# Kernel tuning notes

Hardware: AMD Instinct MI355X
Metric: run time of the kernel (lower is better)

Reference implementation:

```python
import jax, jax.numpy as jnp
import numpy as np

D_MODEL = 1024
NUM_HEADS = 16
D_K = D_MODEL // NUM_HEADS


def setup_inputs() -> dict:
    key = jax.random.key(0)
    ks = jax.random.split(key, 9)
    s = 1.0 / np.sqrt(D_MODEL)
    x = jax.random.normal(ks[0], (2, 2048, D_MODEL), dtype=jnp.float32)
    Wq = jax.random.uniform(ks[1], (D_MODEL, D_MODEL), jnp.float32, -s, s)
    bq = jax.random.uniform(ks[2], (D_MODEL,), jnp.float32, -s, s)
    Wk = jax.random.uniform(ks[3], (D_MODEL, D_MODEL), jnp.float32, -s, s)
    bk = jax.random.uniform(ks[4], (D_MODEL,), jnp.float32, -s, s)
    Wv = jax.random.uniform(ks[5], (D_MODEL, D_MODEL), jnp.float32, -s, s)
    bv = jax.random.uniform(ks[6], (D_MODEL,), jnp.float32, -s, s)
    Wo = jax.random.uniform(ks[7], (D_MODEL, D_MODEL), jnp.float32, -s, s)
    bo = jax.random.uniform(ks[8], (D_MODEL,), jnp.float32, -s, s)
    return {"x": x, "Wq": Wq, "bq": bq, "Wk": Wk, "bk": bk,
            "Wv": Wv, "bv": bv, "Wo": Wo, "bo": bo}


def reference(x, Wq, bq, Wk, bk, Wv, bv, Wo, bo):
    B, S, _ = x.shape
    # projections (torch Linear: x @ W.T + b; here W stored as [in, out])
    q = (x @ Wq + bq).reshape(B, S, NUM_HEADS, D_K).transpose(0, 2, 1, 3)
    k = (x @ Wk + bk).reshape(B, S, NUM_HEADS, D_K).transpose(0, 2, 1, 3)
    v = (x @ Wv + bv).reshape(B, S, NUM_HEADS, D_K).transpose(0, 2, 1, 3)
    scores = jnp.einsum('bhqd,bhkd->bhqk', q, k) / jnp.sqrt(jnp.float32(D_K))
    attn = jax.nn.softmax(scores, axis=-1)
    out = jnp.einsum('bhqk,bhkd->bhqd', attn, v)  # [B,H,S,Dk]
    out = out.transpose(0, 2, 1, 3).reshape(B, S, D_MODEL)
    return out @ Wo + bo
```

## Files before the change

kernel.cpp:

```cpp
#include <hip/hip_runtime.h>
#include <hip/hip_bf16.h>

#define SEQ   2048
#define DM    1024
#define NH    16
#define DK    64
#define BATCH 2
#define M_TOT 4096
#define C1 0.18033688011112042f

typedef __attribute__((ext_vector_type(8))) short bf16x8;
typedef __attribute__((ext_vector_type(4))) float f32x4;
typedef __attribute__((ext_vector_type(16))) float f32x16;
typedef __attribute__((ext_vector_type(2))) int i32x2;
typedef unsigned short u16;

__device__ inline u16 f2b(float f) {
    union { float f; unsigned u; } x; x.f = f;
    return (u16)((x.u + 0x7FFFu + ((x.u >> 16) & 1u)) >> 16);
}

__device__ inline unsigned pk2(float a, float b) {
    __hip_bfloat162 h = __float22bfloat162_rn(make_float2(a, b));
    return *reinterpret_cast<unsigned*>(&h);
}

__device__ inline void async_cp16(const u16* g, u16* l) {
    __builtin_amdgcn_global_load_lds(
        (const __attribute__((address_space(1))) unsigned int*)g,
        (__attribute__((address_space(3))) unsigned int*)l, 16, 0, 0);
}

__device__ inline f32x16 zero16() {
    f32x16 z;
    #pragma unroll
    for (int i = 0; i < 16; ++i) z[i] = 0.f;
    return z;
}

__device__ inline bf16x8 mk8(unsigned a, unsigned b, unsigned c, unsigned d) {
    union { unsigned u[4]; bf16x8 v; } x;
    x.u[0] = a; x.u[1] = b; x.u[2] = c; x.u[3] = d;
    return x.v;
}

#define MFMA32(a, b, c) __builtin_amdgcn_mfma_f32_32x32x16_bf16(a, b, c, 0, 0, 0)

__global__ __launch_bounds__(256) void cast_x(
    const float4* __restrict__ x, uint2* __restrict__ xb)
{
    int gid = blockIdx.x * 256 + threadIdx.x;
    float4 v = x[gid];
    uint2 o;
    o.x = pk2(v.x, v.y); o.y = pk2(v.z, v.w);
    xb[gid] = o;
}

__global__ __launch_bounds__(256) void transpose_cast4(
    const float* __restrict__ W0, const float* __restrict__ W1,
    const float* __restrict__ W2, const float* __restrict__ W3,
    u16* __restrict__ WtBase)
{
    __shared__ float tile[32][33];
    const int t = threadIdx.x;
    const int n0 = blockIdx.x << 5, k0 = blockIdx.y << 5, z = blockIdx.z;
    const float* W = (z == 0) ? W0 : (z == 1) ? W1 : (z == 2) ? W2 : W3;
    u16* Wt = WtBase + (size_t)z * DM * DM;
    #pragma unroll
    for (int i = 0; i < 4; ++i) {
        int idx = t + (i << 8); int r = idx >> 5, c = idx & 31;
        tile[r][c] = W[(size_t)(k0 + r) * DM + n0 + c];
    }
    __syncthreads();
    #pragma unroll
    for (int i = 0; i < 4; ++i) {
        int idx = t + (i << 8); int r = idx >> 5, c = idx & 31;
        Wt[(size_t)(n0 + r) * DM + k0 + c] = f2b(tile[c][r]);
    }
}

__global__ __launch_bounds__(256) void gemm_bt(
    const u16* __restrict__ A, const u16* __restrict__ Bt, int mode,
    const float* __restrict__ bias0, const float* __restrict__ bias1,
    const float* __restrict__ bias2,
    void* __restrict__ out0, void* __restrict__ out1, void* __restrict__ out2)
{
    __shared__ u16 sh[16896];
    u16* As = sh;
    u16* Bs = sh + 8192;
    const int t = threadIdx.x, wid = t >> 6, lane = t & 63;
    const int lr = lane & 15, quad = lane >> 4;
    const int m0 = blockIdx.y << 7, n0 = blockIdx.x << 7;
    const int wm = (wid & 1) << 6, wn = (wid >> 1) << 6;
    const int rowA = lane >> 2;
    const int colA = (((lane & 3) - ((lane >> 3) & 3)) & 3) << 3;
    const int sA = (((lr >> 1) + quad) & 3) << 3;

    f32x4 acc[4][4];
    #pragma unroll
    for (int i = 0; i < 4; ++i)
        #pragma unroll
        for (int j = 0; j < 4; ++j) acc[i][j] = (f32x4){0.f, 0.f, 0.f, 0.f};

    auto stage = [&](int k0s, int buf) {
        #pragma unroll
        for (int i = 0; i < 2; ++i) {
            int ch = wid * 2 + i;
            async_cp16(A  + (size_t)(m0 + ch * 16 + rowA) * DM + k0s + colA,
                       As + buf * 4096 + ch * 16 * 32);
            async_cp16(Bt + (size_t)(n0 + ch * 16 + rowA) * DM + k0s + colA,
                       Bs + buf * 4096 + ch * 16 * 32);
        }
    };

    stage(0, 0);
    __syncthreads();

    for (int k0 = 0; k0 < DM; k0 += 32) {
        const int cur = (k0 >> 5) & 1;
        if (k0 + 32 < DM) stage(k0 + 32, cur ^ 1);

        const u16* Ac = As + cur * 4096;
        const u16* Bc = Bs + cur * 4096;
        bf16x8 af[4], bfr[4];
        #pragma unroll
        for (int mt = 0; mt < 4; ++mt)
            af[mt] = *(const bf16x8*)(Ac + (wm + 16 * mt + lr) * 32 + sA);
        #pragma unroll
        for (int nt = 0; nt < 4; ++nt)
            bfr[nt] = *(const bf16x8*)(Bc + (wn + 16 * nt + lr) * 32 + sA);
        #pragma unroll
        for (int mt = 0; mt < 4; ++mt)
            #pragma unroll
            for (int nt = 0; nt < 4; ++nt)
                acc[mt][nt] = __builtin_amdgcn_mfma_f32_16x16x32_bf16(
                    af[mt], bfr[nt], acc[mt][nt], 0, 0, 0);
        __syncthreads();
    }

    if (mode == 1) {
        u16* wstrip = sh + wid * 1152;
        const int ngb = n0 + wn;
        const int which = ngb >> 10, nnb = ngb & 1023;
        const int h = nnb >> 6;
        const float* bp = (which == 0) ? bias0 : (which == 1) ? bias1 : bias2;
        const float sc = (which == 0) ? C1 : 1.0f;
        float bias_v[4];
        #pragma unroll
        for (int nt = 0; nt < 4; ++nt) bias_v[nt] = bp[nnb + 16 * nt + lr];

        if (which != 1) {
            u16* dst = (which == 0) ? (u16*)out0 : (u16*)out2;
            #pragma unroll
            for (int mt = 0; mt < 4; ++mt) {
                #pragma unroll
                for (int nt = 0; nt < 4; ++nt) {
                    uint2 w;
                    w.x = pk2((acc[mt][nt][0] + bias_v[nt]) * sc,
                              (acc[mt][nt][1] + bias_v[nt]) * sc);
                    w.y = pk2((acc[mt][nt][2] + bias_v[nt]) * sc,
                              (acc[mt][nt][3] + bias_v[nt]) * sc);
                    *(uint2*)(wstrip + (16 * nt + lr) * 16 + quad * 4) = w;
                }
                asm volatile("s_waitcnt lgkmcnt(0)" ::: "memory");
                #pragma unroll
                for (int half = 0; half < 2; ++half) {
                    int id = lane + 64 * half;
                    int d = id >> 1, cho = (id & 1) << 3;
                    int m = m0 + wm + 16 * mt + cho;
                    int b = m >> 11, s = m & (SEQ - 1);
                    *(uint4*)(dst + ((size_t)(b * NH + h) * DK + d) * SEQ + s) =
                        *(const uint4*)(wstrip + d * 16 + cho);
                }
                asm volatile("s_waitcnt lgkmcnt(0)" ::: "memory");
            }
        } else {
            u16* dst = (u16*)out1;
            #pragma unroll
            for (int mt = 0; mt < 4; ++mt) {
                #pragma unroll
                for (int nt = 0; nt < 4; ++nt)
                    #pragma unroll
                    for (int r = 0; r < 4; ++r)
                        wstrip[(quad * 4 + r) * 72 + 16 * nt + lr] =
                            f2b(acc[mt][nt][r] + bias_v[nt]);
                asm volatile("s_waitcnt lgkmcnt(0)" ::: "memory");
                #pragma unroll
                for (int half = 0; half < 2; ++half) {
                    int id = lane + 64 * half;
                    int mloc = id >> 3, dl = (id & 7) << 3;
                    int m = m0 + wm + 16 * mt + mloc;
                    int b = m >> 11, s = m & (SEQ - 1);
                    *(uint4*)(dst + ((size_t)(b * NH + h) * SEQ + s) * DK + dl) =
                        *(const uint4*)(wstrip + mloc * 72 + dl);
                }
                asm volatile("s_waitcnt lgkmcnt(0)" ::: "memory");
            }
        }
    } else {
        float* O = (float*)out0;
        float* strip = (float*)sh + wid * 1088;
        float bias_v[4];
        #pragma unroll
        for (int nt = 0; nt < 4; ++nt) bias_v[nt] = bias0[n0 + wn + 16 * nt + lr];
        #pragma unroll
        for (int mt = 0; mt < 4; ++mt) {
            #pragma unroll
            for (int nt = 0; nt < 4; ++nt)
                #pragma unroll
                for (int r = 0; r < 4; ++r)
                    strip[(quad * 4 + r) * 68 + 16 * nt + lr] =
                        acc[mt][nt][r] + bias_v[nt];
            asm volatile("s_waitcnt lgkmcnt(0)" ::: "memory");
            #pragma unroll
            for (int rr = 0; rr < 4; ++rr) {
                int row = lane >> 2, chunk = (lane & 3) + 4 * rr;
                float4 v = *(const float4*)(strip + row * 68 + chunk * 4);
                *(float4*)(O + (size_t)(m0 + wm + 16 * mt + row) * DM
                             + n0 + wn + chunk * 4) = v;
            }
            asm volatile("s_waitcnt lgkmcnt(0)" ::: "memory");
        }
    }
}

__global__ __launch_bounds__(512) void attn_mfma(
    const u16* __restrict__ Qt, const u16* __restrict__ K,
    const u16* __restrict__ Vt, u16* __restrict__ A)
{
    __shared__ u16 sh[33280];

    const int t = threadIdx.x, wid = t >> 6, lane = t & 63;
    const int l31 = lane & 31, hi = lane >> 5, l7 = lane & 7;
    const int g = wid >> 2, wq = wid & 3;
    const int bx = blockIdx.x;
    const int xcd = bx & 7, within = bx >> 3;
    const int bh  = xcd * 4 + (within >> 4);
    const int q0  = (within & 15) << 7;

    const u16* Kb = K  + (size_t)bh * SEQ * DK;
    const u16* Vb = Vt + (size_t)bh * DK * SEQ;

    const int qw = q0 + 32 * wq + l31;
    const u16* Qb = Qt + (size_t)bh * DK * SEQ + qw;
    bf16x8 bQ[4];
    #pragma unroll
    for (int s = 0; s < 4; ++s)
        #pragma unroll
        for (int j = 0; j < 8; ++j)
            bQ[s][j] = (short)Qb[(size_t)(16 * s + 8 * hi + j) * SEQ];

    f32x16 O0 = zero16(), O1 = zero16();
    float lr = 0.f;

    const int w8row = wid * 8 + (lane >> 3);
    const int scol  = ((l7 ^ (lane >> 3)) << 3);

    const int rA = l31 * 64;
    int cks[4];
    #pragma unroll
    for (int s = 0; s < 4; ++s) cks[s] = ((2 * s + hi) ^ l7) << 3;

    auto stage = [&](int sit, int buf) {
        const int kt = sit << 7;
        u16* kd = sh + (buf << 13) + wid * 512;
        u16* vd = sh + 16384 + (buf << 13) + wid * 512;
        async_cp16(Kb + (size_t)(kt + w8row) * DK + scol,       kd);
        async_cp16(Kb + (size_t)(kt + 64 + w8row) * DK + scol,  kd + 4096);
        async_cp16(Vb + (size_t)w8row * SEQ + kt + scol,        vd);
        async_cp16(Vb + (size_t)w8row * SEQ + kt + 64 + scol,   vd + 4096);
    };

    stage(0, 0);
    __syncthreads();

    for (int sit = 0; sit < SEQ / 128; ++sit) {
        const u16* kbp = sh + ((sit & 1) << 13) + (g << 12) + rA;
        const u16* vbp = sh + 16384 + ((sit & 1) << 13) + (g << 12) + rA;
        if (sit + 1 < SEQ / 128) stage(sit + 1, (sit + 1) & 1);

        f32x16 Sv[2];
        __builtin_amdgcn_s_setprio(1);
        {
            bf16x8 a;
            Sv[0] = zero16();
            a = *(const bf16x8*)(kbp + cks[0]); Sv[0] = MFMA32(a, bQ[0], Sv[0]);
            a = *(const bf16x8*)(kbp + cks[1]); Sv[0] = MFMA32(a, bQ[1], Sv[0]);
            a = *(const bf16x8*)(kbp + cks[2]); Sv[0] = MFMA32(a, bQ[2], Sv[0]);
            a = *(const bf16x8*)(kbp + cks[3]); Sv[0] = MFMA32(a, bQ[3], Sv[0]);
            Sv[1] = zero16();
            a = *(const bf16x8*)(kbp + 2048 + cks[0]); Sv[1] = MFMA32(a, bQ[0], Sv[1]);
            a = *(const bf16x8*)(kbp + 2048 + cks[1]); Sv[1] = MFMA32(a, bQ[1], Sv[1]);
            a = *(const bf16x8*)(kbp + 2048 + cks[2]); Sv[1] = MFMA32(a, bQ[2], Sv[1]);
            a = *(const bf16x8*)(kbp + 2048 + cks[3]); Sv[1] = MFMA32(a, bQ[3], Sv[1]);
        }
        __builtin_amdgcn_s_setprio(0);

        unsigned pa[4][4];
        #pragma unroll
        for (int kvt = 0; kvt < 2; ++kvt) {
            float e[16];
            #pragma unroll
            for (int r = 0; r < 16; ++r)
                e[r] = __builtin_amdgcn_exp2f(Sv[kvt][r]);
            lr += (((e[0] + e[1]) + (e[2] + e[3])) +
                   ((e[4] + e[5]) + (e[6] + e[7]))) +
                  (((e[8] + e[9]) + (e[10] + e[11])) +
                   ((e[12] + e[13]) + (e[14] + e[15])));
            unsigned pk8[8];
            #pragma unroll
            for (int i = 0; i < 8; ++i) pk8[i] = pk2(e[2 * i], e[2 * i + 1]);
            #pragma unroll
            for (int ww = 0; ww < 2; ++ww) {
                i32x2 r0 = __builtin_amdgcn_permlane32_swap(
                    (int)pk8[4 * ww + 0], (int)pk8[4 * ww + 2], false, false);
                i32x2 r1 = __builtin_amdgcn_permlane32_swap(
                    (int)pk8[4 * ww + 1], (int)pk8[4 * ww + 3], false, false);
                const int w = 2 * kvt + ww;
                pa[w][0] = (unsigned)r0[0]; pa[w][1] = (unsigned)r1[0];
                pa[w][2] = (unsigned)r0[1]; pa[w][3] = (unsigned)r1[1];
            }
        }

        __builtin_amdgcn_s_setprio(1);
        #pragma unroll
        for (int w = 0; w < 4; ++w) {
            bf16x8 pw = mk8(pa[w][0], pa[w][1], pa[w][2], pa[w][3]);
            bf16x8 v0 = *(const bf16x8*)(vbp + cks[w]);
            bf16x8 v1 = *(const bf16x8*)(vbp + 2048 + cks[w]);
            O0 = MFMA32(pw, v0, O0);
            O1 = MFMA32(pw, v1, O1);
        }
        __builtin_amdgcn_s_setprio(0);

        __syncthreads();
    }

    lr += __shfl_xor(lr, 32);

    float* lred = (float*)(sh + 32768);
    if (g == 1) {
        float* red = (float*)sh + wq * 2048;
        #pragma unroll
        for (int c = 0; c < 4; ++c) {
            float4 v0 = make_float4(O0[4*c], O0[4*c+1], O0[4*c+2], O0[4*c+3]);
            float4 v1 = make_float4(O1[4*c], O1[4*c+1], O1[4*c+2], O1[4*c+3]);
            *(float4*)(red + lane * 32 + ((c ^ l7) << 2))       = v0;
            *(float4*)(red + lane * 32 + (((c + 4) ^ l7) << 2)) = v1;
        }
        if (hi == 0) lred[wq * 32 + l31] = lr;
    }
    __syncthreads();

    if (g == 0) {
        float* red = (float*)sh + wq * 2048;
        #pragma unroll
        for (int c = 0; c < 4; ++c) {
            float4 v0 = *(const float4*)(red + lane * 32 + ((c ^ l7) << 2));
            float4 v1 = *(const float4*)(red + lane * 32 + (((c + 4) ^ l7) << 2));
            O0[4*c] += v0.x; O0[4*c+1] += v0.y; O0[4*c+2] += v0.z; O0[4*c+3] += v0.w;
            O1[4*c] += v1.x; O1[4*c+1] += v1.y; O1[4*c+2] += v1.z; O1[4*c+3] += v1.w;
        }
        lr += lred[wq * 32 + l31];

        float* lt = (float*)(sh + 33024) + wq * 32;
        lt[l31] = lr;
        asm volatile("s_waitcnt lgkmcnt(0)" ::: "memory");

        const int b = bh >> 4, h = bh & 15;
        u16* Ab = A + (size_t)b * SEQ * DM + h * DK + l31;
        #pragma unroll
        for (int r = 0; r < 16; ++r) {
            const int qr = (r & 3) + 8 * (r >> 2) + 4 * hi;
            const float inv = 1.f / lt[qr];
            u16* dst = Ab + (size_t)(q0 + 32 * wq + qr) * DM;
            dst[0]  = f2b(O0[r] * inv);
            dst[32] = f2b(O1[r] * inv);
        }
    }
}

extern "C" void kernel_launch(void* const* d_in, const int* in_sizes, int n_in,
                              void* d_out, int out_size, void* d_ws, size_t ws_size,
                              hipStream_t stream)
{
    const float* x  = (const float*)d_in[0];
    const float* Wq = (const float*)d_in[1];
    const float* bq = (const float*)d_in[2];
    const float* Wk = (const float*)d_in[3];
    const float* bk = (const float*)d_in[4];
    const float* Wv = (const float*)d_in[5];
    const float* bv = (const float*)d_in[6];
    const float* Wo = (const float*)d_in[7];
    const float* bo = (const float*)d_in[8];

    const size_t NE = (size_t)M_TOT * DM;
    u16* xb     = (u16*)d_ws;
    u16* wt_qkv = xb + NE;
    u16* wt_o   = wt_qkv + 3 * (size_t)DM * DM;
    u16* qt_ws  = wt_o + (size_t)DM * DM;
    u16* k_ws   = qt_ws + NE;
    u16* vt_ws  = k_ws + NE;
    u16* a_ws   = vt_ws + NE;

    cast_x<<<M_TOT * DM / 4 / 256, 256, 0, stream>>>((const float4*)x, (uint2*)xb);
    transpose_cast4<<<dim3(32, 32, 4), 256, 0, stream>>>(Wq, Wk, Wv, Wo, wt_qkv);

    gemm_bt<<<dim3(24, 32), 256, 0, stream>>>(
        xb, wt_qkv, 1, bq, bk, bv, qt_ws, k_ws, vt_ws);

    attn_mfma<<<dim3(512), 512, 0, stream>>>(qt_ws, k_ws, vt_ws, a_ws);

    gemm_bt<<<dim3(8, 32), 256, 0, stream>>>(
        a_ws, wt_o, 0, bo, nullptr, nullptr, d_out, nullptr, nullptr);
}
```

Baseline: 191.2 us.

## Split attention KV range across four wave groups and load V from global

The attention kernel moves to 1024 threads per block, with four wave groups each handling a quarter of every 256-key tile instead of two groups per 128-key tile. K is still staged through double-buffered LDS, but V fragments are now read straight from global memory into registers, which removes V's LDS staging. The partial O accumulators and row sums from the four groups are combined through a two-step LDS reduction. This aims to raise parallelism and cut LDS traffic, at the cost of higher register pressure under the 1024-thread launch bound, uncoalesced global V loads, and extra synchronisation during the reduction.

Result: slower. 601.6 us (+214.6%).

```diff
diff --git a/kernel.cpp b/kernel.cpp
--- a/kernel.cpp
+++ b/kernel.cpp
@@ -42,6 +42,10 @@
     union { unsigned u[4]; bf16x8 v; } x;
     x.u[0] = a; x.u[1] = b; x.u[2] = c; x.u[3] = d;
     return x.v;
+}
+
+__device__ inline bf16x8 u4bf(uint4 v) {
+    union { uint4 u; bf16x8 b; } x; x.u = v; return x.b;
 }
 
 #define MFMA32(a, b, c) __builtin_amdgcn_mfma_f32_32x32x16_bf16(a, b, c, 0, 0, 0)
@@ -224,11 +228,11 @@
     }
 }
 
-__global__ __launch_bounds__(512) void attn_mfma(
+__global__ __launch_bounds__(1024, 8) void attn_mfma(
     const u16* __restrict__ Qt, const u16* __restrict__ K,
     const u16* __restrict__ Vt, u16* __restrict__ A)
 {
-    __shared__ u16 sh[33280];
+    __shared__ u16 sh[34048];
 
     const int t = threadIdx.x, wid = t >> 6, lane = t & 63;
     const int l31 = lane & 31, hi = lane >> 5, l7 = lane & 7;
@@ -251,10 +255,11 @@
             bQ[s][j] = (short)Qb[(size_t)(16 * s + 8 * hi + j) * SEQ];
 
     f32x16 O0 = zero16(), O1 = zero16();
+    const f32x16 Z = zero16();
     float lr = 0.f;
 
-    const int w8row = wid * 8 + (lane >> 3);
-    const int scol  = ((l7 ^ (lane >> 3)) << 3);
+    const int srow = t >> 3;
+    const int scol = ((t & 7) ^ (srow & 7)) << 3;
 
     const int rA = l31 * 64;
     int cks[4];
@@ -262,34 +267,42 @@
     for (int s = 0; s < 4; ++s) cks[s] = ((2 * s + hi) ^ l7) << 3;
 
     auto stage = [&](int sit, int buf) {
-        const int kt = sit << 7;
-        u16* kd = sh + (buf << 13) + wid * 512;
-        u16* vd = sh + 16384 + (buf << 13) + wid * 512;
-        async_cp16(Kb + (size_t)(kt + w8row) * DK + scol,       kd);
-        async_cp16(Kb + (size_t)(kt + 64 + w8row) * DK + scol,  kd + 4096);
-        async_cp16(Vb + (size_t)w8row * SEQ + kt + scol,        vd);
-        async_cp16(Vb + (size_t)w8row * SEQ + kt + 64 + scol,   vd + 4096);
+        const int kt = sit << 8;
+        u16* kd = sh + (buf << 14) + t * 8;
+        async_cp16(Kb + (size_t)(kt + srow) * DK + scol,       kd);
+        async_cp16(Kb + (size_t)(kt + 128 + srow) * DK + scol, kd + 8192);
     };
 
+    const u16* vp0 = Vb + (size_t)l31 * SEQ + 64 * g + 8 * hi;
+    const u16* vp1 = vp0 + (size_t)32 * SEQ;
+
     stage(0, 0);
     __syncthreads();
 
-    for (int sit = 0; sit < SEQ / 128; ++sit) {
-        const u16* kbp = sh + ((sit & 1) << 13) + (g << 12) + rA;
-        const u16* vbp = sh + 16384 + ((sit & 1) << 13) + (g << 12) + rA;
-        if (sit + 1 < SEQ / 128) stage(sit + 1, (sit + 1) & 1);
+    for (int sit = 0; sit < SEQ / 256; ++sit) {
+        const u16* kbp = sh + ((sit & 1) << 14) + (g << 12) + rA;
+        if (sit + 1 < SEQ / 256) stage(sit + 1, (sit + 1) & 1);
+
+        uint4 vld0[4], vld1[4];
+        {
+            const u16* pv0 = vp0 + (sit << 8);
+            const u16* pv1 = vp1 + (sit << 8);
+            #pragma unroll
+            for (int w = 0; w < 4; ++w) {
+                vld0[w] = *(const uint4*)(pv0 + 16 * w);
+                vld1[w] = *(const uint4*)(pv1 + 16 * w);
+            }
+        }
 
         f32x16 Sv[2];
         __builtin_amdgcn_s_setprio(1);
         {
             bf16x8 a;
-            Sv[0] = zero16();
-            a = *(const bf16x8*)(kbp + cks[0]); Sv[0] = MFMA32(a, bQ[0], Sv[0]);
-            a = *(const bf16x8*)(kbp + cks[1]); Sv[0] = MFMA32(a, bQ[1], Sv[0]);
-            a = *(const bf16x8*)(kbp + cks[2]); Sv[0] = MFMA32(a, bQ[2], Sv[0]);
-            a = *(const bf16x8*)(kbp + cks[3]); Sv[0] = MFMA32(a, bQ[3], Sv[0]);
-            Sv[1] = zero16();
-            a = *(const bf16x8*)(kbp + 2048 + cks[0]); Sv[1] = MFMA32(a, bQ[0], Sv[1]);
+            a = *(const bf16x8*)(kbp + cks[0]);        Sv[0] = MFMA32(a, bQ[0], Z);
+            a = *(const bf16x8*)(kbp + cks[1]);        Sv[0] = MFMA32(a, bQ[1], Sv[0]);
+            a = *(const bf16x8*)(kbp + cks[2]);        Sv[0] = MFMA32(a, bQ[2], Sv[0]);
+            a = *(const bf16x8*)(kbp + cks[3]);        Sv[0] = MFMA32(a, bQ[3], Sv[0]);
+            a = *(const bf16x8*)(kbp + 2048 + cks[0]); Sv[1] = MFMA32(a, bQ[0], Z);
             a = *(const bf16x8*)(kbp + 2048 + cks[1]); Sv[1] = MFMA32(a, bQ[1], Sv[1]);
             a = *(const bf16x8*)(kbp + 2048 + cks[2]); Sv[1] = MFMA32(a, bQ[2], Sv[1]);
             a = *(const bf16x8*)(kbp + 2048 + cks[3]); Sv[1] = MFMA32(a, bQ[3], Sv[1]);
@@ -326,10 +339,8 @@
         #pragma unroll
         for (int w = 0; w < 4; ++w) {
             bf16x8 pw = mk8(pa[w][0], pa[w][1], pa[w][2], pa[w][3]);
-            bf16x8 v0 = *(const bf16x8*)(vbp + cks[w]);
-            bf16x8 v1 = *(const bf16x8*)(vbp + 2048 + cks[w]);
-            O0 = MFMA32(pw, v0, O0);
-            O1 = MFMA32(pw, v1, O1);
+            O0 = MFMA32(pw, u4bf(vld0[w]), O0);
+            O1 = MFMA32(pw, u4bf(vld1[w]), O1);
         }
         __builtin_amdgcn_s_setprio(0);
 
@@ -338,9 +349,14 @@
 
     lr += __shfl_xor(lr, 32);
 
-    float* lred = (float*)(sh + 32768);
-    if (g == 1) {
-        float* red = (float*)sh + wq * 2048;
+    float* Ored    = (float*)sh;
+    float* lredAll = (float*)(sh + 32768);
+    float* lt      = (float*)(sh + 33792);
+
+    if (hi == 0) lredAll[(g * 4 + wq) * 32 + l31] = lr;
+
+    auto writeO = [&](int slot) {
+        float* red = Ored + slot * 2048;
         #pragma unroll
         for (int c = 0; c < 4; ++c) {
             float4 v0 = make_float4(O0[4*c], O0[4*c+1], O0[4*c+2], O0[4*c+3]);
@@ -348,12 +364,9 @@
             *(float4*)(red + lane * 32 + ((c ^ l7) << 2))       = v0;
             *(float4*)(red + lane * 32 + (((c + 4) ^ l7) << 2)) = v1;
         }
-        if (hi == 0) lred[wq * 32 + l31] = lr;
-    }
-    __syncthreads();
-
-    if (g == 0) {
-        float* red = (float*)sh + wq * 2048;
+    };
+    auto addO = [&](int slot) {
+        float* red = Ored + slot * 2048;
         #pragma unroll
         for (int c = 0; c < 4; ++c) {
             float4 v0 = *(const float4*)(red + lane * 32 + ((c ^ l7) << 2));
@@ -361,10 +374,21 @@
             O0[4*c] += v0.x; O0[4*c+1] += v0.y; O0[4*c+2] += v0.z; O0[4*c+3] += v0.w;
             O1[4*c] += v1.x; O1[4*c+1] += v1.y; O1[4*c+2] += v1.z; O1[4*c+3] += v1.w;
         }
-        lr += lred[wq * 32 + l31];
-
-        float* lt = (float*)(sh + 33024) + wq * 32;
-        lt[l31] = lr;
+    };
+
+    if (g >= 2) writeO((g - 2) * 4 + wq);
+    __syncthreads();
+    if (g == 0) addO(wq);
+    if (g == 1) addO(4 + wq);
+    __syncthreads();
+    if (g == 1) writeO(wq);
+    __syncthreads();
+
+    if (g == 0) {
+        addO(wq);
+        float ltot = lredAll[wq * 32 + l31] + lredAll[(4 + wq) * 32 + l31]
+                   + lredAll[(8 + wq) * 32 + l31] + lredAll[(12 + wq) * 32 + l31];
+        lt[wq * 32 + l31] = ltot;
         asm volatile("s_waitcnt lgkmcnt(0)" ::: "memory");
 
         const int b = bh >> 4, h = bh & 15;
@@ -372,7 +396,7 @@
         #pragma unroll
         for (int r = 0; r < 16; ++r) {
             const int qr = (r & 3) + 8 * (r >> 2) + 4 * hi;
-            const float inv = 1.f / lt[qr];
+            const float inv = 1.f / lt[wq * 32 + qr];
             u16* dst = Ab + (size_t)(q0 + 32 * wq + qr) * DM;
             dst[0]  = f2b(O0[r] * inv);
             dst[32] = f2b(O1[r] * inv);
@@ -409,7 +433,7 @@
     gemm_bt<<<dim3(24, 32), 256, 0, stream>>>(
         xb, wt_qkv, 1, bq, bk, bv, qt_ws, k_ws, vt_ws);
 
-    attn_mfma<<<dim3(512), 512, 0, stream>>>(qt_ws, k_ws, vt_ws, a_ws);
+    attn_mfma<<<dim3(512), 1024, 0, stream>>>(qt_ws, k_ws, vt_ws, a_ws);
 
     gemm_bt<<<dim3(8, 32), 256, 0, stream>>>(
         a_ws, wt_o, 0, bo, nullptr, nullptr, d_out, nullptr, nullptr);
```
